# Optimization experiments

Hardware: AMD Instinct MI355X
Metric: run time of the kernel (lower is better)

## Reference

```python
import jax, jax.numpy as jnp
import numpy as np

N, LATENT, K, C = 50000, 16, 16, 64
BATCH = 4
MU = 2.0
HOT_TEMP = 0.01  # sigmoid temperature in hotness()


def _linear_init(key, out_dim, in_dim):
    s = 1.0 / np.sqrt(in_dim)
    kw, kb = jax.random.split(key)
    w = jax.random.uniform(kw, (out_dim, in_dim), jnp.float32, -s, s)
    b = jax.random.uniform(kb, (out_dim,), jnp.float32, -s, s)
    return w, b


def setup_inputs() -> dict:
    key = jax.random.key(0)
    ks = jax.random.split(key, 10)
    x = jax.random.normal(ks[0], (BATCH, N), jnp.float32)
    neighbour_id = jax.random.randint(ks[1], (N, K), 0, N)
    neighbour_distance = jax.random.uniform(ks[2], (N, K), jnp.float32)
    # self-neighbor at distance 0 (as in a real kNN table); keeps window sums > 0
    neighbour_distance = neighbour_distance.at[:, 0].set(0.0)
    clustering_labels = jax.random.randint(ks[3], (N,), 0, C)
    enc1_w, enc1_b = _linear_init(ks[4], 200, N)
    enc2_w, enc2_b = _linear_init(ks[5], LATENT, 200)
    dec_w, dec_b = _linear_init(ks[6], N, LATENT)
    h0_w, h0_b = _linear_init(ks[7], 200, LATENT)
    h1_w, h1_b = _linear_init(ks[8], 200, 200)
    h2_w, h2_b = _linear_init(ks[9], C, 200)
    B = jnp.array([1.0], jnp.float32)  # learnable bandwidth scale, B0=1.0
    return dict(x=x, neighbour_id=neighbour_id, neighbour_distance=neighbour_distance,
                clustering_labels=clustering_labels, enc1_w=enc1_w, enc1_b=enc1_b,
                enc2_w=enc2_w, enc2_b=enc2_b, dec_w=dec_w, dec_b=dec_b,
                h0_w=h0_w, h0_b=h0_b, h1_w=h1_w, h1_b=h1_b, h2_w=h2_w, h2_b=h2_b, B=B)


def reference(x, neighbour_id, neighbour_distance, clustering_labels,
              enc1_w, enc1_b, enc2_w, enc2_b, dec_w, dec_b,
              h0_w, h0_b, h1_w, h1_b, h2_w, h2_b, B):
    # ---- encode: Linear(N,200) -> sigmoid -> Linear(200,n)
    h = jax.nn.sigmoid(x @ enc1_w.T + enc1_b)
    encoded = h @ enc2_w.T + enc2_b                      # [b, n]

    # ---- hotness MLP (SiLU hidden layers, soft sigmoid output), batched over b
    z = encoded @ h0_w.T + h0_b
    z = z * jax.nn.sigmoid(z)
    z = z @ h1_w.T + h1_b
    z = z * jax.nn.sigmoid(z)
    z = z @ h2_w.T + h2_b                                # [b, C]
    H_cluster = jax.nn.sigmoid(HOT_TEMP * z)             # 1/(1+exp(-0.01 z))
    H = H_cluster[:, clustering_labels]                  # [b, N]

    # ---- per-mode bandwidths: (1 - H/2)^i * B,  i = 0..n-1
    powers = jnp.arange(LATENT, dtype=jnp.float32)[:, None]   # [n, 1]
    w = (1.0 - H[:, None, :] / 2.0) ** powers * B[0]          # [b, n, N]

    # ---- bubble window over K neighbours, normalized over K
    d2 = neighbour_distance ** 2                              # [N, K]
    denom = (w * MU) ** 2                                     # [b, n, N]
    win = jax.nn.relu(1.0 - d2[None, None] / denom[..., None])  # [b, n, N, K]
    win = win / jnp.sum(win, axis=-1, keepdims=True)

    # ---- convolve decoder basis (decoder.weight.T is [n, N]) with window
    basis_nbrs = dec_w.T[:, neighbour_id]                     # [n, N, K] gather
    convolved = jnp.einsum('bnik,nik->bni', win, basis_nbrs)  # [b, n, N]

    # ---- decode: bmm(encoded[b,1,n], convolved[b,n,N]) + bias
    out = jnp.einsum('bn,bni->bi', encoded, convolved) + dec_b  # [b, N]
    return out
```

## Files before the change

kernel.cpp:

```cpp
#include <hip/hip_runtime.h>
#include <math.h>

#define NPTS 50000
#define KNBR 16
#define LAT  16
#define NCLS 64
#define NB   4

#define ENC1_CHUNKS 5
#define ENC1_BLOCKS (200 * ENC1_CHUNKS)
#define NLANES (NPTS * 4)
#define CONV_BLOCKS ((NLANES + 255) / 256)

__device__ __forceinline__ float sigmoidf_(float v) { return 1.0f / (1.0f + expf(-v)); }

__global__ __launch_bounds__(256) void k_enc1(const float* __restrict__ x,
                                              const float* __restrict__ w,
                                              float* __restrict__ part) {
  const int NV4 = NPTS / 4;
  const int CV  = NV4 / ENC1_CHUNKS;
  int bid = blockIdx.x;
  int j = bid / ENC1_CHUNKS;
  int chunk = bid - j * ENC1_CHUNKS;
  int t = threadIdx.x;
  const float4* wv = (const float4*)(w + (size_t)j * NPTS);
  const float4* xv = (const float4*)x;
  float a0 = 0.f, a1 = 0.f, a2 = 0.f, a3 = 0.f;
  int vend = (chunk + 1) * CV;
#pragma unroll 2
  for (int v = chunk * CV + t; v < vend; v += 256) {
    float4 wf = wv[v];
    float4 x0 = xv[v];
    float4 x1 = xv[NV4 + v];
    float4 x2 = xv[2 * NV4 + v];
    float4 x3 = xv[3 * NV4 + v];
    a0 += wf.x * x0.x + wf.y * x0.y + wf.z * x0.z + wf.w * x0.w;
    a1 += wf.x * x1.x + wf.y * x1.y + wf.z * x1.z + wf.w * x1.w;
    a2 += wf.x * x2.x + wf.y * x2.y + wf.z * x2.z + wf.w * x2.w;
    a3 += wf.x * x3.x + wf.y * x3.y + wf.z * x3.z + wf.w * x3.w;
  }
#pragma unroll
  for (int off = 32; off > 0; off >>= 1) {
    a0 += __shfl_down(a0, off);
    a1 += __shfl_down(a1, off);
    a2 += __shfl_down(a2, off);
    a3 += __shfl_down(a3, off);
  }
  __shared__ float red[4][4];
  int wid = t >> 6;
  if ((t & 63) == 0) {
    red[wid][0] = a0; red[wid][1] = a1; red[wid][2] = a2; red[wid][3] = a3;
  }
  __syncthreads();
  if (t < 4) {
    float s = red[0][t] + red[1][t] + red[2][t] + red[3][t];
    part[j * 20 + chunk * 4 + t] = s;
  }
}

__global__ __launch_bounds__(1024) void k_mlp(const float* __restrict__ part,
                                              const float* __restrict__ enc1_b,
                                              const float* __restrict__ enc2_w,
                                              const float* __restrict__ enc2_b,
                                              const float* __restrict__ h0_w,
                                              const float* __restrict__ h0_b,
                                              const float* __restrict__ h1_w,
                                              const float* __restrict__ h1_b,
                                              const float* __restrict__ h2_w,
                                              const float* __restrict__ h2_b,
                                              float* __restrict__ w_enc,
                                              float* __restrict__ w_hcl) {
  __shared__ float s_h[NB][200];
  __shared__ float s_enc[NB][LAT];
  __shared__ __align__(16) float s_z0t[200][NB];
  __shared__ __align__(16) float s_z1t[200][NB];
  int t = threadIdx.x;

  if (t < 800) {
    int j = t >> 2, b = t & 3;
    float v = part[j * 20 + 0 + b] + part[j * 20 + 4 + b] + part[j * 20 + 8 + b] +
              part[j * 20 + 12 + b] + part[j * 20 + 16 + b] + enc1_b[j];
    s_h[b][j] = sigmoidf_(v);
  }
  __syncthreads();

  {
    int g = t >> 4, p = t & 15;
    int b = g >> 4, i = g & 15;
    const float4* w4 = (const float4*)(enc2_w + i * 200);
    float s = 0.f;
    for (int f = p; f < 50; f += 16) {
      float4 w = w4[f];
      int j = f * 4;
      s += w.x * s_h[b][j] + w.y * s_h[b][j + 1] + w.z * s_h[b][j + 2] + w.w * s_h[b][j + 3];
    }
    s += __shfl_xor(s, 1, 16);
    s += __shfl_xor(s, 2, 16);
    s += __shfl_xor(s, 4, 16);
    s += __shfl_xor(s, 8, 16);
    if (p == 0) {
      s += enc2_b[i];
      s_enc[b][i] = s;
      w_enc[b * LAT + i] = s;
    }
  }
  __syncthreads();

  if (t < 800) {
    int jo = t >> 2, b = t & 3;
    const float4* hw = (const float4*)(h0_w + jo * LAT);
    float4 w0 = hw[0], w1 = hw[1], w2 = hw[2], w3 = hw[3];
    float s = h0_b[jo];
    s += w0.x * s_enc[b][0] + w0.y * s_enc[b][1] + w0.z * s_enc[b][2] + w0.w * s_enc[b][3];
    s += w1.x * s_enc[b][4] + w1.y * s_enc[b][5] + w1.z * s_enc[b][6] + w1.w * s_enc[b][7];
    s += w2.x * s_enc[b][8] + w2.y * s_enc[b][9] + w2.z * s_enc[b][10] + w2.w * s_enc[b][11];
    s += w3.x * s_enc[b][12] + w3.y * s_enc[b][13] + w3.z * s_enc[b][14] + w3.w * s_enc[b][15];
    s_z0t[jo][b] = s * sigmoidf_(s);
  }
  __syncthreads();

  if (t < 800) {
    int r = t >> 2, q = t & 3;
    const float4* w4 = (const float4*)(h1_w + r * 200);
    float d0 = 0.f, d1 = 0.f, d2 = 0.f, d3 = 0.f;
    for (int f = q; f < 50; f += 4) {
      float4 w = w4[f];
      int j = f * 4;
      float4 z0 = *(const float4*)&s_z0t[j][0];
      float4 z1 = *(const float4*)&s_z0t[j + 1][0];
      float4 z2 = *(const float4*)&s_z0t[j + 2][0];
      float4 z3 = *(const float4*)&s_z0t[j + 3][0];
      d0 += w.x * z0.x + w.y * z1.x + w.z * z2.x + w.w * z3.x;
      d1 += w.x * z0.y + w.y * z1.y + w.z * z2.y + w.w * z3.y;
      d2 += w.x * z0.z + w.y * z1.z + w.z * z2.z + w.w * z3.z;
      d3 += w.x * z0.w + w.y * z1.w + w.z * z2.w + w.w * z3.w;
    }
    d0 += __shfl_xor(d0, 1, 4); d0 += __shfl_xor(d0, 2, 4);
    d1 += __shfl_xor(d1, 1, 4); d1 += __shfl_xor(d1, 2, 4);
    d2 += __shfl_xor(d2, 1, 4); d2 += __shfl_xor(d2, 2, 4);
    d3 += __shfl_xor(d3, 1, 4); d3 += __shfl_xor(d3, 2, 4);
    if (q == 0) {
      float bb = h1_b[r];
      float sa;
      sa = d0 + bb; s_z1t[r][0] = sa * sigmoidf_(sa);
      sa = d1 + bb; s_z1t[r][1] = sa * sigmoidf_(sa);
      sa = d2 + bb; s_z1t[r][2] = sa * sigmoidf_(sa);
      sa = d3 + bb; s_z1t[r][3] = sa * sigmoidf_(sa);
    }
  }
  __syncthreads();

  {
    int c = t >> 4, p = t & 15;
    const float4* w4 = (const float4*)(h2_w + c * 200);
    float e0 = 0.f, e1 = 0.f, e2 = 0.f, e3 = 0.f;
    for (int f = p; f < 50; f += 16) {
      float4 w = w4[f];
      int j = f * 4;
      float4 za = *(const float4*)&s_z1t[j][0];
      float4 zb = *(const float4*)&s_z1t[j + 1][0];
      float4 zc = *(const float4*)&s_z1t[j + 2][0];
      float4 zd = *(const float4*)&s_z1t[j + 3][0];
      e0 += w.x * za.x + w.y * zb.x + w.z * zc.x + w.w * zd.x;
      e1 += w.x * za.y + w.y * zb.y + w.z * zc.y + w.w * zd.y;
      e2 += w.x * za.z + w.y * zb.z + w.z * zc.z + w.w * zd.z;
      e3 += w.x * za.w + w.y * zb.w + w.z * zc.w + w.w * zd.w;
    }
#pragma unroll
    for (int m = 8; m > 0; m >>= 1) {
      e0 += __shfl_xor(e0, m, 16);
      e1 += __shfl_xor(e1, m, 16);
      e2 += __shfl_xor(e2, m, 16);
      e3 += __shfl_xor(e3, m, 16);
    }
    if (p == 0) {
      float sb = h2_b[c];
      w_hcl[0 * NCLS + c] = sigmoidf_(0.01f * (e0 + sb));
      w_hcl[1 * NCLS + c] = sigmoidf_(0.01f * (e1 + sb));
      w_hcl[2 * NCLS + c] = sigmoidf_(0.01f * (e2 + sb));
      w_hcl[3 * NCLS + c] = sigmoidf_(0.01f * (e3 + sb));
    }
  }
}

__global__ __launch_bounds__(256) void k_conv(const int* __restrict__ nid,
                                              const float* __restrict__ nd,
                                              const int* __restrict__ labels,
                                              const float* __restrict__ dec_w,
                                              const float* __restrict__ dec_b,
                                              const float* __restrict__ Bp,
                                              const float* __restrict__ w_enc,
                                              const float* __restrict__ w_hcl,
                                              float* __restrict__ out) {
  __shared__ float s_enc[NB * LAT];
  __shared__ float s_hcl[NB * NCLS];
  int t = threadIdx.x;
  if (t < NB * LAT) s_enc[t] = w_enc[t];
  s_hcl[t] = w_hcl[t];
  __syncthreads();

  int gidx = blockIdx.x * 256 + t;
  int n = gidx >> 2;
  int q = t & 3;
  if (n >= NPTS) return;

  const float4* nd4 = (const float4*)nd + (size_t)n * 4;
  const int4*   ni4 = (const int4*)nid + (size_t)n * 4;
  float dA[16];
  int nA[16];
#pragma unroll
  for (int a = 0; a < 4; ++a) {
    float4 v = nd4[a];
    int4  iv = ni4[a];
    dA[a * 4 + 0] = v.x * v.x; dA[a * 4 + 1] = v.y * v.y;
    dA[a * 4 + 2] = v.z * v.z; dA[a * 4 + 3] = v.w * v.w;
    nA[a * 4 + 0] = iv.x; nA[a * 4 + 1] = iv.y;
    nA[a * 4 + 2] = iv.z; nA[a * 4 + 3] = iv.w;
  }

  int lab = labels[n];
  float decb = dec_b[n];
  float Bv = Bp[0];

  const float4* dw4 = (const float4*)dec_w;
  float4 dwp[8];
#pragma unroll
  for (int k = 0; k < 8; ++k)
    dwp[k] = dw4[(size_t)nA[k] * 4 + q];

  float inv0 = 1.0f / (4.0f * Bv * Bv);

  float ivd[4][4];
#pragma unroll
  for (int b = 0; b < 4; ++b) {
    float H = s_hcl[b * NCLS + lab];
    float base = 1.0f - 0.5f * H;
    float rb = __builtin_amdgcn_rcpf(base * base);
    float rb2 = rb * rb;
    float rb4 = rb2 * rb2;
    float rb8 = rb4 * rb4;
    float start = inv0;
    if (q & 1) start *= rb4;
    if (q & 2) start *= rb8;
    ivd[b][0] = start;
    ivd[b][1] = ivd[b][0] * rb;
    ivd[b][2] = ivd[b][1] * rb;
    ivd[b][3] = ivd[b][2] * rb;
  }

  float sden[4][4], num[4][4];
#pragma unroll
  for (int b = 0; b < 4; ++b)
#pragma unroll
    for (int j = 0; j < 4; ++j) { sden[b][j] = 0.f; num[b][j] = 0.f; }

#pragma unroll
  for (int k = 0; k < KNBR; ++k) {
    float4 dw = (k < 8) ? dwp[k] : dw4[(size_t)nA[k] * 4 + q];
    float d2k = dA[k];
#pragma unroll
    for (int b = 0; b < 4; ++b) {
      float w0 = fmaxf(fmaf(-d2k, ivd[b][0], 1.0f), 0.0f);
      float w1 = fmaxf(fmaf(-d2k, ivd[b][1], 1.0f), 0.0f);
      float w2 = fmaxf(fmaf(-d2k, ivd[b][2], 1.0f), 0.0f);
      float w3 = fmaxf(fmaf(-d2k, ivd[b][3], 1.0f), 0.0f);
      sden[b][0] += w0; num[b][0] = fmaf(w0, dw.x, num[b][0]);
      sden[b][1] += w1; num[b][1] = fmaf(w1, dw.y, num[b][1]);
      sden[b][2] += w2; num[b][2] = fmaf(w2, dw.z, num[b][2]);
      sden[b][3] += w3; num[b][3] = fmaf(w3, dw.w, num[b][3]);
    }
  }

  float acc[4];
#pragma unroll
  for (int b = 0; b < 4; ++b) {
    float a = 0.f;
#pragma unroll
    for (int j = 0; j < 4; ++j) {
      a = fmaf(s_enc[b * LAT + q * 4 + j] * __builtin_amdgcn_rcpf(sden[b][j]),
               num[b][j], a);
    }
    acc[b] = a;
  }

  float tA = (q & 1) ? acc[0] : acc[2];
  float tB = (q & 1) ? acc[1] : acc[3];
  float rA = __shfl_xor(tA, 1, 4);
  float rB = __shfl_xor(tB, 1, 4);
  float u = (q & 1) ? (acc[2] + rA) : (acc[0] + rA);
  float v = (q & 1) ? (acc[3] + rB) : (acc[1] + rB);
  float tC = (q & 2) ? u : v;
  float rC = __shfl_xor(tC, 2, 4);
  float f = (q & 2) ? (v + rC) : (u + rC);
  int bmap = ((q & 1) << 1) | ((q & 2) >> 1);
  out[(size_t)bmap * NPTS + n] = f + decb;
}

extern "C" void kernel_launch(void* const* d_in, const int* in_sizes, int n_in,
                              void* d_out, int out_size, void* d_ws, size_t ws_size,
                              hipStream_t stream) {
  const float* x      = (const float*)d_in[0];
  const int*   nid    = (const int*)d_in[1];
  const float* nd     = (const float*)d_in[2];
  const int*   labels = (const int*)d_in[3];
  const float* enc1_w = (const float*)d_in[4];
  const float* enc1_b = (const float*)d_in[5];
  const float* enc2_w = (const float*)d_in[6];
  const float* enc2_b = (const float*)d_in[7];
  const float* dec_w  = (const float*)d_in[8];
  const float* dec_b  = (const float*)d_in[9];
  const float* h0_w   = (const float*)d_in[10];
  const float* h0_b   = (const float*)d_in[11];
  const float* h1_w   = (const float*)d_in[12];
  const float* h1_b   = (const float*)d_in[13];
  const float* h2_w   = (const float*)d_in[14];
  const float* h2_b   = (const float*)d_in[15];
  const float* Bp     = (const float*)d_in[16];
  float* out = (float*)d_out;
  float* ws  = (float*)d_ws;
  float* part  = ws;
  float* w_enc = ws + 4000;
  float* w_hcl = ws + 4064;

  k_enc1<<<ENC1_BLOCKS, 256, 0, stream>>>(x, enc1_w, part);
  k_mlp<<<1, 1024, 0, stream>>>(part, enc1_b, enc2_w, enc2_b, h0_w, h0_b,
                                h1_w, h1_b, h2_w, h2_b, w_enc, w_hcl);
  k_conv<<<CONV_BLOCKS, 256, 0, stream>>>(nid, nd, labels, dec_w, dec_b,
                                          Bp, w_enc, w_hcl, out);
}
```

Baseline: 39.59 us.

## Split conv neighbour loop across two lane halves with shuffle reduction

The convolution kernel now uses 8 lanes per point instead of 4, and each half handles 8 of the 16 neighbours. All 8 gathers per lane are issued up front, and the partial window sums and numerators are combined with xor-4 shuffles before the existing per-batch reduction. This doubles thread count and memory-level parallelism for the random dec_w gathers, while shortening each thread's serial chain. In exchange it adds 32 shuffles per lane, and half the lanes recompute the bandwidth setup only to discard it at the store.

```diff
diff --git a/kernel.cpp b/kernel.cpp
--- a/kernel.cpp
+++ b/kernel.cpp
@@ -9,8 +9,8 @@
 
 #define ENC1_CHUNKS 5
 #define ENC1_BLOCKS (200 * ENC1_CHUNKS)
-#define NLANES (NPTS * 4)
-#define CONV_BLOCKS ((NLANES + 255) / 256)
+#define NLANES8 (NPTS * 8)
+#define CONV_BLOCKS ((NLANES8 + 255) / 256)
 
 __device__ __forceinline__ float sigmoidf_(float v) { return 1.0f / (1.0f + expf(-v)); }
 
@@ -200,23 +200,22 @@
   __syncthreads();
 
   int gidx = blockIdx.x * 256 + t;
-  int n = gidx >> 2;
-  int q = t & 3;
+  int n = gidx >> 3;
+  int p = t & 7;
+  int half = p >> 2;
+  int q = p & 3;
   if (n >= NPTS) return;
 
-  const float4* nd4 = (const float4*)nd + (size_t)n * 4;
-  const int4*   ni4 = (const int4*)nid + (size_t)n * 4;
-  float dA[16];
-  int nA[16];
-#pragma unroll
-  for (int a = 0; a < 4; ++a) {
-    float4 v = nd4[a];
-    int4  iv = ni4[a];
-    dA[a * 4 + 0] = v.x * v.x; dA[a * 4 + 1] = v.y * v.y;
-    dA[a * 4 + 2] = v.z * v.z; dA[a * 4 + 3] = v.w * v.w;
-    nA[a * 4 + 0] = iv.x; nA[a * 4 + 1] = iv.y;
-    nA[a * 4 + 2] = iv.z; nA[a * 4 + 3] = iv.w;
-  }
+  const float4* nd4 = (const float4*)nd + (size_t)n * 4 + half * 2;
+  const int4*   ni4 = (const int4*)nid + (size_t)n * 4 + half * 2;
+  float4 v0 = nd4[0], v1 = nd4[1];
+  int4  i0 = ni4[0], i1 = ni4[1];
+  float dA[8];
+  int nA[8];
+  dA[0] = v0.x * v0.x; dA[1] = v0.y * v0.y; dA[2] = v0.z * v0.z; dA[3] = v0.w * v0.w;
+  dA[4] = v1.x * v1.x; dA[5] = v1.y * v1.y; dA[6] = v1.z * v1.z; dA[7] = v1.w * v1.w;
+  nA[0] = i0.x; nA[1] = i0.y; nA[2] = i0.z; nA[3] = i0.w;
+  nA[4] = i1.x; nA[5] = i1.y; nA[6] = i1.z; nA[7] = i1.w;
 
   int lab = labels[n];
   float decb = dec_b[n];
@@ -255,8 +254,8 @@
     for (int j = 0; j < 4; ++j) { sden[b][j] = 0.f; num[b][j] = 0.f; }
 
 #pragma unroll
-  for (int k = 0; k < KNBR; ++k) {
-    float4 dw = (k < 8) ? dwp[k] : dw4[(size_t)nA[k] * 4 + q];
+  for (int k = 0; k < 8; ++k) {
+    float4 dw = dwp[k];
     float d2k = dA[k];
 #pragma unroll
     for (int b = 0; b < 4; ++b) {
@@ -268,6 +267,15 @@
       sden[b][1] += w1; num[b][1] = fmaf(w1, dw.y, num[b][1]);
       sden[b][2] += w2; num[b][2] = fmaf(w2, dw.z, num[b][2]);
       sden[b][3] += w3; num[b][3] = fmaf(w3, dw.w, num[b][3]);
+    }
+  }
+
+#pragma unroll
+  for (int b = 0; b < 4; ++b) {
+#pragma unroll
+    for (int j = 0; j < 4; ++j) {
+      sden[b][j] += __shfl_xor(sden[b][j], 4, 8);
+      num[b][j]  += __shfl_xor(num[b][j], 4, 8);
     }
   }
 
@@ -293,7 +301,7 @@
   float rC = __shfl_xor(tC, 2, 4);
   float f = (q & 2) ? (v + rC) : (u + rC);
   int bmap = ((q & 1) << 1) | ((q & 2) >> 1);
-  out[(size_t)bmap * NPTS + n] = f + decb;
+  if (half == 0) out[(size_t)bmap * NPTS + n] = f + decb;
 }
 
 extern "C" void kernel_launch(void* const* d_in, const int* in_sizes, int n_in,
```

After: 40.72 us. 1.03x slower.

## Split single-block MLP into multi-block kernels for hidden layers

Applied to the files above, without the earlier changes.

Splits the single-block MLP kernel into three kernels: the first computes the encoder and first hidden layer, then the 200x200 layer runs across 50 blocks and the output layer across 16 blocks, each row reduced by one wavefront. The goal is to spread the weight loads and dot products of the serial single-block stage over many compute units. In exchange, it adds two kernel launches and passes the intermediates through global memory.

```diff
diff --git a/kernel.cpp b/kernel.cpp
--- a/kernel.cpp
+++ b/kernel.cpp
@@ -58,22 +58,16 @@
   }
 }
 
-__global__ __launch_bounds__(1024) void k_mlp(const float* __restrict__ part,
-                                              const float* __restrict__ enc1_b,
-                                              const float* __restrict__ enc2_w,
-                                              const float* __restrict__ enc2_b,
-                                              const float* __restrict__ h0_w,
-                                              const float* __restrict__ h0_b,
-                                              const float* __restrict__ h1_w,
-                                              const float* __restrict__ h1_b,
-                                              const float* __restrict__ h2_w,
-                                              const float* __restrict__ h2_b,
-                                              float* __restrict__ w_enc,
-                                              float* __restrict__ w_hcl) {
+__global__ __launch_bounds__(1024) void k_mlpABC(const float* __restrict__ part,
+                                                 const float* __restrict__ enc1_b,
+                                                 const float* __restrict__ enc2_w,
+                                                 const float* __restrict__ enc2_b,
+                                                 const float* __restrict__ h0_w,
+                                                 const float* __restrict__ h0_b,
+                                                 float* __restrict__ w_enc,
+                                                 float* __restrict__ z0g) {
   __shared__ float s_h[NB][200];
   __shared__ float s_enc[NB][LAT];
-  __shared__ __align__(16) float s_z0t[200][NB];
-  __shared__ __align__(16) float s_z1t[200][NB];
   int t = threadIdx.x;
 
   if (t < 800) {
@@ -115,71 +109,82 @@
     s += w1.x * s_enc[b][4] + w1.y * s_enc[b][5] + w1.z * s_enc[b][6] + w1.w * s_enc[b][7];
     s += w2.x * s_enc[b][8] + w2.y * s_enc[b][9] + w2.z * s_enc[b][10] + w2.w * s_enc[b][11];
     s += w3.x * s_enc[b][12] + w3.y * s_enc[b][13] + w3.z * s_enc[b][14] + w3.w * s_enc[b][15];
-    s_z0t[jo][b] = s * sigmoidf_(s);
-  }
-  __syncthreads();
-
-  if (t < 800) {
-    int r = t >> 2, q = t & 3;
-    const float4* w4 = (const float4*)(h1_w + r * 200);
-    float d0 = 0.f, d1 = 0.f, d2 = 0.f, d3 = 0.f;
-    for (int f = q; f < 50; f += 4) {
-      float4 w = w4[f];
-      int j = f * 4;
-      float4 z0 = *(const float4*)&s_z0t[j][0];
-      float4 z1 = *(const float4*)&s_z0t[j + 1][0];
-      float4 z2 = *(const float4*)&s_z0t[j + 2][0];
-      float4 z3 = *(const float4*)&s_z0t[j + 3][0];
-      d0 += w.x * z0.x + w.y * z1.x + w.z * z2.x + w.w * z3.x;
-      d1 += w.x * z0.y + w.y * z1.y + w.z * z2.y + w.w * z3.y;
-      d2 += w.x * z0.z + w.y * z1.z + w.z * z2.z + w.w * z3.z;
-      d3 += w.x * z0.w + w.y * z1.w + w.z * z2.w + w.w * z3.w;
-    }
-    d0 += __shfl_xor(d0, 1, 4); d0 += __shfl_xor(d0, 2, 4);
-    d1 += __shfl_xor(d1, 1, 4); d1 += __shfl_xor(d1, 2, 4);
-    d2 += __shfl_xor(d2, 1, 4); d2 += __shfl_xor(d2, 2, 4);
-    d3 += __shfl_xor(d3, 1, 4); d3 += __shfl_xor(d3, 2, 4);
-    if (q == 0) {
-      float bb = h1_b[r];
-      float sa;
-      sa = d0 + bb; s_z1t[r][0] = sa * sigmoidf_(sa);
-      sa = d1 + bb; s_z1t[r][1] = sa * sigmoidf_(sa);
-      sa = d2 + bb; s_z1t[r][2] = sa * sigmoidf_(sa);
-      sa = d3 + bb; s_z1t[r][3] = sa * sigmoidf_(sa);
-    }
-  }
-  __syncthreads();
-
-  {
-    int c = t >> 4, p = t & 15;
-    const float4* w4 = (const float4*)(h2_w + c * 200);
-    float e0 = 0.f, e1 = 0.f, e2 = 0.f, e3 = 0.f;
-    for (int f = p; f < 50; f += 16) {
-      float4 w = w4[f];
-      int j = f * 4;
-      float4 za = *(const float4*)&s_z1t[j][0];
-      float4 zb = *(const float4*)&s_z1t[j + 1][0];
-      float4 zc = *(const float4*)&s_z1t[j + 2][0];
-      float4 zd = *(const float4*)&s_z1t[j + 3][0];
-      e0 += w.x * za.x + w.y * zb.x + w.z * zc.x + w.w * zd.x;
-      e1 += w.x * za.y + w.y * zb.y + w.z * zc.y + w.w * zd.y;
-      e2 += w.x * za.z + w.y * zb.z + w.z * zc.z + w.w * zd.z;
-      e3 += w.x * za.w + w.y * zb.w + w.z * zc.w + w.w * zd.w;
-    }
-#pragma unroll
-    for (int m = 8; m > 0; m >>= 1) {
-      e0 += __shfl_xor(e0, m, 16);
-      e1 += __shfl_xor(e1, m, 16);
-      e2 += __shfl_xor(e2, m, 16);
-      e3 += __shfl_xor(e3, m, 16);
-    }
-    if (p == 0) {
-      float sb = h2_b[c];
-      w_hcl[0 * NCLS + c] = sigmoidf_(0.01f * (e0 + sb));
-      w_hcl[1 * NCLS + c] = sigmoidf_(0.01f * (e1 + sb));
-      w_hcl[2 * NCLS + c] = sigmoidf_(0.01f * (e2 + sb));
-      w_hcl[3 * NCLS + c] = sigmoidf_(0.01f * (e3 + sb));
-    }
+    z0g[jo * 4 + b] = s * sigmoidf_(s);
+  }
+}
+
+__global__ __launch_bounds__(256) void k_mlpD(const float* __restrict__ z0g,
+                                              const float* __restrict__ h1_w,
+                                              const float* __restrict__ h1_b,
+                                              float* __restrict__ z1g) {
+  __shared__ __align__(16) float4 s_z0[200];
+  int t = threadIdx.x;
+  for (int o = t; o < 200; o += 256) s_z0[o] = ((const float4*)z0g)[o];
+  __syncthreads();
+
+  int row = blockIdx.x * 4 + (t >> 6);
+  int l = t & 63;
+  float d0 = 0.f, d1 = 0.f, d2 = 0.f, d3 = 0.f;
+  if (l < 50) {
+    float4 w = ((const float4*)(h1_w + row * 200))[l];
+    float4 z0 = s_z0[4 * l + 0], z1 = s_z0[4 * l + 1];
+    float4 z2 = s_z0[4 * l + 2], z3 = s_z0[4 * l + 3];
+    d0 = w.x * z0.x + w.y * z1.x + w.z * z2.x + w.w * z3.x;
+    d1 = w.x * z0.y + w.y * z1.y + w.z * z2.y + w.w * z3.y;
+    d2 = w.x * z0.z + w.y * z1.z + w.z * z2.z + w.w * z3.z;
+    d3 = w.x * z0.w + w.y * z1.w + w.z * z2.w + w.w * z3.w;
+  }
+#pragma unroll
+  for (int m = 32; m > 0; m >>= 1) {
+    d0 += __shfl_xor(d0, m, 64);
+    d1 += __shfl_xor(d1, m, 64);
+    d2 += __shfl_xor(d2, m, 64);
+    d3 += __shfl_xor(d3, m, 64);
+  }
+  if (l == 0) {
+    float bb = h1_b[row];
+    float s;
+    s = d0 + bb; z1g[row * 4 + 0] = s * sigmoidf_(s);
+    s = d1 + bb; z1g[row * 4 + 1] = s * sigmoidf_(s);
+    s = d2 + bb; z1g[row * 4 + 2] = s * sigmoidf_(s);
+    s = d3 + bb; z1g[row * 4 + 3] = s * sigmoidf_(s);
+  }
+}
+
+__global__ __launch_bounds__(256) void k_mlpE(const float* __restrict__ z1g,
+                                              const float* __restrict__ h2_w,
+                                              const float* __restrict__ h2_b,
+                                              float* __restrict__ w_hcl) {
+  __shared__ __align__(16) float4 s_z1[200];
+  int t = threadIdx.x;
+  for (int o = t; o < 200; o += 256) s_z1[o] = ((const float4*)z1g)[o];
+  __syncthreads();
+
+  int c = blockIdx.x * 4 + (t >> 6);
+  int l = t & 63;
+  float e0 = 0.f, e1 = 0.f, e2 = 0.f, e3 = 0.f;
+  if (l < 50) {
+    float4 w = ((const float4*)(h2_w + c * 200))[l];
+    float4 za = s_z1[4 * l + 0], zb = s_z1[4 * l + 1];
+    float4 zc = s_z1[4 * l + 2], zd = s_z1[4 * l + 3];
+    e0 = w.x * za.x + w.y * zb.x + w.z * zc.x + w.w * zd.x;
+    e1 = w.x * za.y + w.y * zb.y + w.z * zc.y + w.w * zd.y;
+    e2 = w.x * za.z + w.y * zb.z + w.z * zc.z + w.w * zd.z;
+    e3 = w.x * za.w + w.y * zb.w + w.z * zc.w + w.w * zd.w;
+  }
+#pragma unroll
+  for (int m = 32; m > 0; m >>= 1) {
+    e0 += __shfl_xor(e0, m, 64);
+    e1 += __shfl_xor(e1, m, 64);
+    e2 += __shfl_xor(e2, m, 64);
+    e3 += __shfl_xor(e3, m, 64);
+  }
+  if (l == 0) {
+    float sb = h2_b[c];
+    w_hcl[0 * NCLS + c] = sigmoidf_(0.01f * (e0 + sb));
+    w_hcl[1 * NCLS + c] = sigmoidf_(0.01f * (e1 + sb));
+    w_hcl[2 * NCLS + c] = sigmoidf_(0.01f * (e2 + sb));
+    w_hcl[3 * NCLS + c] = sigmoidf_(0.01f * (e3 + sb));
   }
 }
 
@@ -321,10 +326,14 @@
   float* part  = ws;
   float* w_enc = ws + 4000;
   float* w_hcl = ws + 4064;
+  float* z0g   = ws + 4320;
+  float* z1g   = ws + 5120;
 
   k_enc1<<<ENC1_BLOCKS, 256, 0, stream>>>(x, enc1_w, part);
-  k_mlp<<<1, 1024, 0, stream>>>(part, enc1_b, enc2_w, enc2_b, h0_w, h0_b,
-                                h1_w, h1_b, h2_w, h2_b, w_enc, w_hcl);
+  k_mlpABC<<<1, 1024, 0, stream>>>(part, enc1_b, enc2_w, enc2_b, h0_w, h0_b,
+                                   w_enc, z0g);
+  k_mlpD<<<50, 256, 0, stream>>>(z0g, h1_w, h1_b, z1g);
+  k_mlpE<<<16, 256, 0, stream>>>(z1g, h2_w, h2_b, w_hcl);
   k_conv<<<CONV_BLOCKS, 256, 0, stream>>>(nid, nd, labels, dec_w, dec_b,
                                           Bp, w_enc, w_hcl, out);
 }
```

After: 37.76 us. 4.6% less time.
